# Kernel tuning notes

Hardware: AMD Instinct MI355X
Metric: run time of the kernel (lower is better)

Reference implementation:

```python
import jax, jax.numpy as jnp
import numpy as np

B, S, D = 128, 256, 768          # batch, seq (pre-sentinel), encoder dim
ARC, TAG = 500, 100              # arc / tag representation dims
LAYERS, TOPK = 2, 8              # config['gnn_layers'], config['top_k']
SP = S + 1                       # seq_len after head sentinel


def setup_inputs() -> dict:
    key = jax.random.key(0)
    ks = jax.random.split(key, 32)
    sc = 0.02
    inp = {
        'inputs': jax.random.normal(ks[0], (B, S, D), jnp.float32),
        'tag_embeddings': jax.random.randint(ks[1], (B, S), 0, 50),
        'mask': jnp.ones((B, S), jnp.int32),
        'head_indices': jax.random.randint(ks[2], (B, S), 0, S),
        'head_tags': jax.random.randint(ks[3], (B, S), 0, 50),
        # parameters
        'head_sentinel': jax.random.normal(ks[4], (D,), jnp.float32),
        'W_ha': jax.random.normal(ks[5], (D, ARC)) * sc, 'b_ha': jnp.zeros((ARC,)),
        'W_da': jax.random.normal(ks[6], (D, ARC)) * sc, 'b_da': jnp.zeros((ARC,)),
        'W_ht': jax.random.normal(ks[7], (D, TAG)) * sc, 'b_ht': jnp.zeros((TAG,)),
        'W_dt': jax.random.normal(ks[8], (D, TAG)) * sc, 'b_dt': jnp.zeros((TAG,)),
        # bilinear attention: use_input_biases=True -> (ARC+1, ARC+1), plus scalar bias
        'bil_W': jax.random.normal(ks[9], (LAYERS + 1, ARC + 1, ARC + 1)) * sc,
        'bil_b': jnp.zeros((LAYERS + 1,)),
        # GCNConv params (PyG: x @ W, symmetric-normalized aggregate, + bias)
        'c1a_W': jax.random.normal(ks[10], (ARC, ARC)) * sc, 'c1a_b': jnp.zeros((ARC,)),
        'c2a_W': jax.random.normal(ks[11], (ARC, ARC)) * sc, 'c2a_b': jnp.zeros((ARC,)),
        'c1r_W': jax.random.normal(ks[12], (TAG, TAG)) * sc, 'c1r_b': jnp.zeros((TAG,)),
        'c2r_W': jax.random.normal(ks[13], (TAG, TAG)) * sc, 'c2r_b': jnp.zeros((TAG,)),
    }
    return inp


def bilinear_attn(m1, m2, W, b):
    # AllenNLP BilinearMatrixAttention with use_input_biases=True
    ones1 = jnp.ones(m1.shape[:-1] + (1,), m1.dtype)
    m1b = jnp.concatenate([m1, ones1], -1)
    m2b = jnp.concatenate([m2, ones1], -1)
    return jnp.einsum('bie,ef,bjf->bij', m1b, W, m2b) + b


def batch_top_k(probs, k):
    # probs: [B, SP, SP] row-softmaxed; edge j(head)->i(dep) for each row's top-k cols,
    # with global (batched) node indexing.
    vals, idx = jax.lax.top_k(probs, k)                      # [B, SP, k]
    offs = (jnp.arange(B) * SP)[:, None, None]
    src = (idx + offs).reshape(-1)
    dst = (jnp.broadcast_to(jnp.arange(SP)[None, :, None], idx.shape) + offs).reshape(-1)
    return src, dst, vals.reshape(-1)


def gcn_conv(x, src, dst, ew, W, b):
    # PyG GCNConv: x@W, add self-loops (weight 1), sym norm, scatter-add at dst, + bias
    N = x.shape[0]
    x = x @ W
    loop = jnp.arange(N)
    row = jnp.concatenate([src, loop])
    col = jnp.concatenate([dst, loop])
    w = jnp.concatenate([ew, jnp.ones((N,), x.dtype)])
    deg = jax.ops.segment_sum(w, col, num_segments=N)
    dinv = jnp.where(deg > 0, jax.lax.rsqrt(deg), 0.0)
    norm = dinv[row] * w * dinv[col]
    out = jax.ops.segment_sum(x[row] * norm[:, None], col, num_segments=N)
    return out + b


def reference(inputs, tag_embeddings, mask, head_indices, head_tags,
              head_sentinel, W_ha, b_ha, W_da, b_da, W_ht, b_ht, W_dt, b_dt,
              bil_W, bil_b, c1a_W, c1a_b, c2a_W, c2a_b, c1r_W, c1r_b, c2r_W, c2r_b):
    elu = jax.nn.elu
    x = jnp.concatenate([jnp.broadcast_to(head_sentinel, (B, 1, D)), inputs], axis=1)  # [B,SP,D]
    head_arc = elu(x @ W_ha + b_ha)
    dept_arc = elu(x @ W_da + b_da)
    head_tag = elu(x @ W_ht + b_ht)
    dep_tag = elu(x @ W_dt + b_dt)

    def two_conv(feat, W1, b1, W2, b2, src, dst, ew):
        h = gcn_conv(feat.reshape(B * SP, -1), src, dst, ew, W1, b1)
        h = gcn_conv(elu(h), src, dst, ew, W2, b2)
        return h.reshape(B, SP, -1)

    for k in range(LAYERS):
        arc_logits = bilinear_attn(head_arc, dept_arc, bil_W[k], bil_b[k])
        arc_probs = jax.nn.softmax(arc_logits, axis=-1)
        src, dst, ew = batch_top_k(arc_probs, TOPK)
        head_arc = two_conv(head_arc, c1a_W, c1a_b, c2a_W, c2a_b, src, dst, ew)
        dept_arc = two_conv(dept_arc, c1a_W, c1a_b, c2a_W, c2a_b, src, dst, ew)
        head_tag = two_conv(head_tag, c1r_W, c1r_b, c2r_W, c2r_b, src, dst, ew)
        dep_tag = two_conv(dep_tag, c1r_W, c1r_b, c2r_W, c2r_b, src, dst, ew)

    arc_logits = bilinear_attn(head_arc, dept_arc, bil_W[-1], bil_b[-1])
    return arc_logits, head_tag, dep_tag
```

## Files before the change

### kernel.cpp

```cpp
#include <hip/hip_runtime.h>
#include <hip/hip_bf16.h>
#include <math.h>
#include <cstddef>

namespace {

constexpr int kB   = 128;
constexpr int kS   = 256;
constexpr int kD   = 768;
constexpr int kSP  = 257;
constexpr int kN   = kB * kSP;
constexpr int kARC = 500;
constexpr int kTAG = 100;
constexpr int KA   = 512;
constexpr int KT   = 128;
constexpr int NPA  = 1024;
constexpr int NPT  = 256;

typedef __attribute__((ext_vector_type(8))) short short8;
typedef __attribute__((ext_vector_type(4))) float floatx4;
typedef __attribute__((ext_vector_type(2))) float floatx2;
typedef __attribute__((ext_vector_type(4))) unsigned short ushort4v;
typedef __attribute__((ext_vector_type(2))) unsigned short ushort2v;
typedef __hip_bfloat16 bf;

__device__ __forceinline__ float bfval(bf h) { return __bfloat162float(h); }
__device__ __forceinline__ unsigned short bfbits(bf h) {
  unsigned short u; __builtin_memcpy(&u, &h, 2); return u;
}
__device__ __forceinline__ void splitf(float x, bf* h, bf* l) {
  bf hh = __float2bfloat16(x);
  *h = hh;
  *l = __float2bfloat16(x - __bfloat162float(hh));
}

__device__ __forceinline__ int swz8(int lid, int total) {
  int q = total >> 3, r = total & 7;
  int c = lid & 7, p = lid >> 3;
  return (c < r ? c * (q + 1) : r * (q + 1) + (c - r) * q) + p;
}

__device__ __forceinline__ void gload16(const bf* g, bf* l) {
  __builtin_amdgcn_global_load_lds(
      (const __attribute__((address_space(1))) void*)g,
      (__attribute__((address_space(3))) void*)l, 16, 0, 0);
}

__global__ void zerofill(unsigned* __restrict__ p, long n4) {
  long i = (long)blockIdx.x * 256 + threadIdx.x;
  if (i < n4) p[i] = 0u;
}

__global__ void detect_dtype_n(const unsigned* __restrict__ raw, int* __restrict__ flag,
                               int nwords) {
  int lane = threadIdx.x;
  int ok = 0, nz = 0;
  if (lane < nwords) {
    unsigned w = raw[lane];
    if (w != 0u) {
      nz = 1;
      int e = (w >> 7) & 0xFF;
      ok = (e >= 90 && e <= 140);
    }
  }
  unsigned long long ball_ok = __ballot(ok);
  unsigned long long ball_nz = __ballot(nz);
  if (lane == 0) {
    int cok = __popcll(ball_ok), cnz = __popcll(ball_nz);
    flag[0] = (cok * 4 >= cnz * 3) ? 1 : 0;
  }
}

__device__ __forceinline__ float rawload(const void* p, size_t i, int bfm) {
  return bfm ? __bfloat162float(((const bf*)p)[i]) : ((const float*)p)[i];
}

__global__ void conv_off(const void* __restrict__ src, float* __restrict__ dst,
                         int n, long off, const int* __restrict__ flag) {
  int i = blockIdx.x * 256 + threadIdx.x;
  if (i >= n) return;
  dst[i] = rawload(src, (size_t)off + i, *flag);
}

__global__ void wsplit_t(const void* __restrict__ src, const int* __restrict__ flag,
                         long srcOff, int ldsrc, int K, int N, int Kpad,
                         bf* __restrict__ Wh, bf* __restrict__ Wl) {
  long idx = (long)blockIdx.x * 256 + threadIdx.x;
  if (idx >= (long)N * Kpad) return;
  int n = (int)(idx / Kpad), k = (int)(idx % Kpad);
  float v = (k < K) ? rawload(src, (size_t)srcOff + (size_t)k * ldsrc + n, *flag) : 0.f;
  bf h, l;
  splitf(v, &h, &l);
  Wh[idx] = h; Wl[idx] = l;
}

__global__ void xsplit(const void* __restrict__ inp, const void* __restrict__ sent,
                       const int* __restrict__ fi, const int* __restrict__ fs,
                       bf* __restrict__ xh, bf* __restrict__ xl, int g0, int NG) {
  long idx = (long)blockIdx.x * 256 + threadIdx.x;
  long tot = (long)NG * (kD / 4);
  if (idx >= tot) return;
  int n = (int)(idx / (kD / 4));
  int k = (int)(idx % (kD / 4)) * 4;
  int b = n / kSP, r = n - b * kSP;
  const void* src;
  size_t base;
  int bfm;
  if (r == 0) { src = sent; base = (size_t)k; bfm = *fs; }
  else {
    src = inp;
    base = ((size_t)((g0 + b) * kS + (r - 1))) * kD + k;
    bfm = *fi;
  }
  float v[4];
  if (bfm) {
    ushort4v s = *(const ushort4v*)((const unsigned short*)src + base);
#pragma unroll
    for (int j = 0; j < 4; ++j) {
      bf h; unsigned short u = s[j];
      __builtin_memcpy(&h, &u, 2);
      v[j] = __bfloat162float(h);
    }
  } else {
    floatx4 f4 = *(const floatx4*)((const float*)src + base);
#pragma unroll
    for (int j = 0; j < 4; ++j) v[j] = f4[j];
  }
  ushort4v h4, l4;
#pragma unroll
  for (int j = 0; j < 4; ++j) {
    bf h, l;
    splitf(v[j], &h, &l);
    h4[j] = bfbits(h); l4[j] = bfbits(l);
  }
  size_t o = (size_t)n * kD + k;
  *(ushort4v*)((unsigned short*)xh + o) = h4;
  *(ushort4v*)((unsigned short*)xl + o) = l4;
}

constexpr int BM = 128, BN = 128, BK = 32;

template <int EPI, int OUTF32>
__global__ __launch_bounds__(256) void gemm_sp(
    const bf* __restrict__ Ah, const bf* __restrict__ Al, int lda,
    const bf* __restrict__ Bh, const bf* __restrict__ Bl, int ldb,
    bf* __restrict__ Ch, bf* __restrict__ Cl, float* __restrict__ Cf, int ldc,
    int M, int N, int K, const float* __restrict__ bias) {
  __shared__ bf sAh[2][BM][BK];
  __shared__ bf sAl[2][BM][BK];
  __shared__ bf sBh[2][BN][BK];
  __shared__ bf sBl[2][BN][BK];
  const int tid = threadIdx.x;
  const int lane = tid & 63, wave = tid >> 6;
  const int quad = lane >> 4, l15 = lane & 15;
  const int wm = (wave >> 1) * 64, wn = (wave & 1) * 64;
  const int gy = gridDim.y;
  const int sw = swz8(blockIdx.x + blockIdx.y * gridDim.x, gridDim.x * gy);
  const int m0 = (sw / gy) * BM, n0 = (sw % gy) * BN;
  const int lrow = lane >> 2, lkof = (lane & 3) * 8;

  const bf *pAh[2], *pAl[2], *pBh[2], *pBl[2];
  int rb[2];
#pragma unroll
  for (int jj = 0; jj < 2; ++jj) {
    rb[jj] = wave * 32 + jj * 16;
    int gm = m0 + rb[jj] + lrow; if (gm > M - 1) gm = M - 1;
    int gn = n0 + rb[jj] + lrow; if (gn > N - 1) gn = N - 1;
    pAh[jj] = Ah + (size_t)gm * lda + lkof;
    pAl[jj] = Al + (size_t)gm * lda + lkof;
    pBh[jj] = Bh + (size_t)gn * ldb + lkof;
    pBl[jj] = Bl + (size_t)gn * ldb + lkof;
  }

  auto stage = [&](int bi, int k0) {
#pragma unroll
    for (int jj = 0; jj < 2; ++jj) {
      gload16(pAh[jj] + k0, &sAh[bi][rb[jj]][0]);
      gload16(pAl[jj] + k0, &sAl[bi][rb[jj]][0]);
      gload16(pBh[jj] + k0, &sBh[bi][rb[jj]][0]);
      gload16(pBl[jj] + k0, &sBl[bi][rb[jj]][0]);
    }
  };

  floatx4 acc[4][4] = {};
  stage(0, 0);
  int cur = 0;
  for (int k0 = 0; k0 < K; k0 += BK) {
    __syncthreads();
    if (k0 + BK < K) stage(cur ^ 1, k0 + BK);
    short8 a_h[4], a_l[4], b_h[4], b_l[4];
#pragma unroll
    for (int t = 0; t < 4; ++t) {
      a_h[t] = *(const short8*)&sAh[cur][wm + t * 16 + l15][quad * 8];
      a_l[t] = *(const short8*)&sAl[cur][wm + t * 16 + l15][quad * 8];
      b_h[t] = *(const short8*)&sBh[cur][wn + t * 16 + l15][quad * 8];
      b_l[t] = *(const short8*)&sBl[cur][wn + t * 16 + l15][quad * 8];
    }
#pragma unroll
    for (int mt = 0; mt < 4; ++mt)
#pragma unroll
      for (int nt = 0; nt < 4; ++nt) {
        acc[mt][nt] = __builtin_amdgcn_mfma_f32_16x16x32_bf16(a_h[mt], b_h[nt], acc[mt][nt], 0, 0, 0);
        acc[mt][nt] = __builtin_amdgcn_mfma_f32_16x16x32_bf16(a_h[mt], b_l[nt], acc[mt][nt], 0, 0, 0);
        acc[mt][nt] = __builtin_amdgcn_mfma_f32_16x16x32_bf16(a_l[mt], b_h[nt], acc[mt][nt], 0, 0, 0);
      }
    cur ^= 1;
  }
#pragma unroll
  for (int mt = 0; mt < 4; ++mt)
#pragma unroll
    for (int reg = 0; reg < 4; ++reg) {
      int m = m0 + wm + mt * 16 + quad * 4 + reg;
      if (m >= M) continue;
#pragma unroll
      for (int nt = 0; nt < 4; ++nt) {
        int n = n0 + wn + nt * 16 + l15;
        if (OUTF32) {
          if (n < N) {
            float v = acc[mt][nt][reg];
            if (EPI >= 1) v += bias[n];
            if (EPI == 1) v = v > 0.f ? v : expm1f(v);
            Cf[(size_t)m * ldc + n] = v;
          }
        } else {
          size_t o = (size_t)m * ldc + n;
          if (n < N) {
            float v = acc[mt][nt][reg];
            if (EPI >= 1) v += bias[n];
            if (EPI == 1) v = v > 0.f ? v : expm1f(v);
            bf h, l;
            splitf(v, &h, &l);
            Ch[o] = h; Cl[o] = l;
          } else if (n < ldc) {
            Ch[o] = __float2bfloat16(0.f);
            Cl[o] = __float2bfloat16(0.f);
          }
        }
      }
    }
}

__global__ __launch_bounds__(256) void bilnt_sp(
    const bf* __restrict__ Th, const bf* __restrict__ Tl,
    const bf* __restrict__ Fh, const bf* __restrict__ Fl, int ldf,
    float* __restrict__ out, const float* __restrict__ bilb, int bidx,
    int g0, int globOut) {
  __shared__ bf sAh[2][BM][BK];
  __shared__ bf sAl[2][BM][BK];
  __shared__ bf sBh[2][BN][BK];
  __shared__ bf sBl[2][BN][BK];
  const int tid = threadIdx.x;
  const int lane = tid & 63, wave = tid >> 6;
  const int quad = lane >> 4, l15 = lane & 15;
  const int wm = (wave >> 1) * 64, wn = (wave & 1) * 64;
  const int gx = gridDim.x, gxy = gridDim.x * gridDim.y;
  const int sw = swz8(blockIdx.x + gx * blockIdx.y + gxy * blockIdx.z, gxy * gridDim.z);
  const int z = sw / gxy;
  const int rem = sw % gxy;
  const int m0 = (rem % gx) * BM, n0 = (rem / gx) * BN;
  const int lrow = lane >> 2, lkof = (lane & 3) * 8;
  const bf* Ah = Th + (size_t)z * kSP * KA;
  const bf* Al = Tl + (size_t)z * kSP * KA;
  const bf* Bh = Fh + (size_t)z * kSP * ldf;
  const bf* Bl = Fl + (size_t)z * kSP * ldf;

  const bf *pAh[2], *pAl[2], *pBh[2], *pBl[2];
  int rb[2];
#pragma unroll
  for (int jj = 0; jj < 2; ++jj) {
    rb[jj] = wave * 32 + jj * 16;
    int gm = m0 + rb[jj] + lrow; if (gm > kSP - 1) gm = kSP - 1;
    int gn = n0 + rb[jj] + lrow; if (gn > kSP - 1) gn = kSP - 1;
    pAh[jj] = Ah + (size_t)gm * KA + lkof;
    pAl[jj] = Al + (size_t)gm * KA + lkof;
    pBh[jj] = Bh + (size_t)gn * ldf + lkof;
    pBl[jj] = Bl + (size_t)gn * ldf + lkof;
  }

  auto stage = [&](int bi, int k0) {
#pragma unroll
    for (int jj = 0; jj < 2; ++jj) {
      gload16(pAh[jj] + k0, &sAh[bi][rb[jj]][0]);
      gload16(pAl[jj] + k0, &sAl[bi][rb[jj]][0]);
      gload16(pBh[jj] + k0, &sBh[bi][rb[jj]][0]);
      gload16(pBl[jj] + k0, &sBl[bi][rb[jj]][0]);
    }
  };

  floatx4 acc[4][4] = {};
  stage(0, 0);
  int cur = 0;
  for (int k0 = 0; k0 < KA; k0 += BK) {
    __syncthreads();
    if (k0 + BK < KA) stage(cur ^ 1, k0 + BK);
    short8 a_h[4], a_l[4], b_h[4], b_l[4];
#pragma unroll
    for (int t = 0; t < 4; ++t) {
      a_h[t] = *(const short8*)&sAh[cur][wm + t * 16 + l15][quad * 8];
      a_l[t] = *(const short8*)&sAl[cur][wm + t * 16 + l15][quad * 8];
      b_h[t] = *(const short8*)&sBh[cur][wn + t * 16 + l15][quad * 8];
      b_l[t] = *(const short8*)&sBl[cur][wn + t * 16 + l15][quad * 8];
    }
#pragma unroll
    for (int mt = 0; mt < 4; ++mt)
#pragma unroll
      for (int nt = 0; nt < 4; ++nt) {
        acc[mt][nt] = __builtin_amdgcn_mfma_f32_16x16x32_bf16(a_h[mt], b_h[nt], acc[mt][nt], 0, 0, 0);
        acc[mt][nt] = __builtin_amdgcn_mfma_f32_16x16x32_bf16(a_h[mt], b_l[nt], acc[mt][nt], 0, 0, 0);
        acc[mt][nt] = __builtin_amdgcn_mfma_f32_16x16x32_bf16(a_l[mt], b_h[nt], acc[mt][nt], 0, 0, 0);
      }
    cur ^= 1;
  }
  const float sb = bilb[bidx];
  const int bb = globOut ? (g0 + z) : z;
#pragma unroll
  for (int mt = 0; mt < 4; ++mt)
#pragma unroll
    for (int reg = 0; reg < 4; ++reg) {
      int i = m0 + wm + mt * 16 + quad * 4 + reg;
      if (i >= kSP) continue;
      float rowterm = bfval(Ah[(size_t)i * KA + 500]) + bfval(Al[(size_t)i * KA + 500]) + sb;
#pragma unroll
      for (int nt = 0; nt < 4; ++nt) {
        int j = n0 + wn + nt * 16 + l15;
        if (j >= kSP) continue;
        out[((size_t)bb * kSP + i) * kSP + j] = acc[mt][nt][reg] + rowterm;
      }
    }
}

__global__ void softmax_topk(const float* __restrict__ logits,
                             unsigned short* __restrict__ idx8,
                             float* __restrict__ val8,
                             float* __restrict__ dinv) {
  const int row = blockIdx.x;
  const int lane = threadIdx.x;
  const float* L = logits + (size_t)row * kSP;
  float v[5];
  int c[5];
#pragma unroll
  for (int q = 0; q < 5; ++q) {
    int j = lane + q * 64;
    c[q] = j;
    v[q] = (j < kSP) ? L[j] : -INFINITY;
  }
  float m = v[0];
#pragma unroll
  for (int q = 1; q < 5; ++q) m = fmaxf(m, v[q]);
  for (int off = 32; off > 0; off >>= 1) m = fmaxf(m, __shfl_xor(m, off));
  float s = 0.f;
#pragma unroll
  for (int q = 0; q < 5; ++q) s += expf(v[q] - m);
  for (int off = 32; off > 0; off >>= 1) s += __shfl_xor(s, off);
  const float invs = 1.f / s;
  float degsum = 0.f;
  for (int t = 0; t < 8; ++t) {
    float bvv = -INFINITY;
    int bii = 0;
#pragma unroll
    for (int q = 0; q < 5; ++q)
      if (v[q] > bvv) { bvv = v[q]; bii = c[q]; }
    for (int off = 32; off > 0; off >>= 1) {
      float ov = __shfl_xor(bvv, off);
      int oi = __shfl_xor(bii, off);
      if (ov > bvv || (ov == bvv && oi < bii)) { bvv = ov; bii = oi; }
    }
    float p = expf(bvv - m) * invs;
    degsum += p;
    if (lane == 0) { idx8[row * 8 + t] = (unsigned short)bii; val8[row * 8 + t] = p; }
#pragma unroll
    for (int q = 0; q < 5; ++q)
      if (c[q] == bii) v[q] = -INFINITY;
  }
  if (lane == 0) dinv[row] = 1.f / sqrtf(1.f + degsum);
}

template <int ELU, int OUTF32>
__global__ void gcn_agg(const float* __restrict__ Y, int ldy, int F,
                        const unsigned short* __restrict__ idx8,
                        const float* __restrict__ val8,
                        const float* __restrict__ dinv, const float* __restrict__ bias,
                        bf* __restrict__ Zh, bf* __restrict__ Zl,
                        float* __restrict__ Zf, int ldzf, long halfStr) {
  const int r = swz8(blockIdx.x, gridDim.x);
  const int m = r >> 1, p = r & 1;
  __shared__ float w[9];
  __shared__ int srcs[8];
  const int t = threadIdx.x;
  if (t < 8) {
    int b0 = m - (m % kSP);
    int s = b0 + (int)idx8[m * 8 + t];
    srcs[t] = 2 * s + p;
    w[t] = dinv[m] * val8[m * 8 + t] * dinv[s];
  } else if (t == 8) {
    float di = dinv[m];
    w[8] = di * di;
  }
  __syncthreads();
  const int lim = OUTF32 ? F : ldy;
  for (int f = t * 2; f < lim; f += (int)blockDim.x * 2) {
    size_t on = (size_t)r * ldy + f;
    if (!OUTF32 && f >= F) {
      ushort2v zz = {0, 0};
      *(ushort2v*)((unsigned short*)Zh + on) = zz;
      *(ushort2v*)((unsigned short*)Zl + on) = zz;
      continue;
    }
    floatx2 y0 = *(const floatx2*)(Y + on);
    float a0 = w[8] * y0[0], a1 = w[8] * y0[1];
#pragma unroll
    for (int e = 0; e < 8; ++e) {
      floatx2 ys = *(const floatx2*)(Y + (size_t)srcs[e] * ldy + f);
      a0 += w[e] * ys[0];
      a1 += w[e] * ys[1];
    }
    a0 += bias[f];
    a1 += bias[f + 1];
    if (ELU) {
      a0 = a0 > 0.f ? a0 : expm1f(a0);
      a1 = a1 > 0.f ? a1 : expm1f(a1);
    }
    if (OUTF32) {
      float* zp = Zf + (size_t)p * halfStr + (size_t)m * ldzf + f;
      floatx2 o = {a0, a1};
      *(floatx2*)zp = o;
    } else {
      bf h0, l0, h1, l1;
      splitf(a0, &h0, &l0);
      splitf(a1, &h1, &l1);
      ushort2v hv = {bfbits(h0), bfbits(h1)};
      ushort2v lv = {bfbits(l0), bfbits(l1)};
      *(ushort2v*)((unsigned short*)Zh + on) = hv;
      *(ushort2v*)((unsigned short*)Zl + on) = lv;
    }
  }
}

}

extern "C" void kernel_launch(void* const* d_in, const int* in_sizes, int n_in,
                              void* d_out, int out_size, void* d_ws, size_t ws_size,
                              hipStream_t stream) {
  (void)out_size;

  const int roleSize[20] = {kB * kS * kD, kD,
                            kD * kARC, kARC, kD * kARC, kARC,
                            kD * kTAG, kTAG, kD * kTAG, kTAG,
                            3 * 501 * 501, 3,
                            kARC * kARC, kARC, kARC * kARC, kARC,
                            kTAG * kTAG, kTAG, kTAG * kTAG, kTAG};
  const int roleOcc[20]  = {0, 0, 0, 0, 1, 1, 0, 0, 1, 1, 0, 0,
                            0, 2, 1, 3, 0, 2, 1, 3};
  int roleIdx[20] = {0, 5, 6, 7, 8, 9, 10, 11, 12, 13, 14, 15,
                     16, 17, 18, 19, 20, 21, 22, 23};
  for (int r = 0; r < 20; ++r) {
    int occ = 0, found = -1;
    for (int i = 0; i < n_in; ++i) {
      if (in_sizes[i] == roleSize[r]) {
        if (occ == roleOcc[r]) { found = i; break; }
        ++occ;
      }
    }
    if (found >= 0) roleIdx[r] = found;
    else if (roleIdx[r] >= n_in) roleIdx[r] = 0;
  }
  const void* src_of[20];
  for (int r = 0; r < 20; ++r) src_of[r] = d_in[roleIdx[r]];

  auto r1_bytes = [](size_t NG) -> size_t {
    size_t a = (size_t)2 * NG * KA * 4;
    size_t b = NG * kD * 2 * 2;
    size_t c = NG * KA * 2 * 2 + NG * kSP * 4;
    size_t m = a; if (b > m) m = b; if (c > m) m = c;
    return m;
  };
  auto need_bytes = [&](int GB) -> size_t {
    size_t NG = (size_t)GB * kSP, s = 0;
    auto al = [&](size_t b) { s += (b + 255) & ~(size_t)255; };
    al(256);
    al((size_t)NPA * kD * 2); al((size_t)NPA * kD * 2);
    al((size_t)NPT * kD * 2); al((size_t)NPT * kD * 2);
    al(NPA * 4); al(NPT * 4);
    for (int i = 0; i < 6; ++i) al((size_t)501 * KA * 2);
    al(3 * 501 * 4); al(256);
    for (int i = 0; i < 4; ++i) al((size_t)kARC * KA * 2);
    for (int i = 0; i < 4; ++i) al((size_t)kTAG * KT * 2);
    al(kARC * 4); al(kARC * 4); al(kTAG * 4); al(kTAG * 4);
    al(NG * NPA * 2); al(NG * NPA * 2);
    al(NG * NPT * 2); al(NG * NPT * 2);
    al(r1_bytes(NG));
    al((size_t)2 * NG * KA * 2 * 2);
    al(NG * 8 * 2); al(NG * 8 * 4); al(NG * 4);
    return s;
  };
  int GB = 1;
  for (int cand : {128, 64, 32, 16, 8, 4, 2, 1})
    if (need_bytes(cand) <= ws_size) { GB = cand; break; }
  const int G = kB / GB;
  const int NG = GB * kSP;
  const int mb  = (NG + BM - 1) / BM;
  const int mb2 = (2 * NG + BM - 1) / BM;

  char* ws = (char*)d_ws;
  size_t off = 0;
  auto alloc = [&](size_t bytes) -> void* {
    void* p = ws + off;
    off += (bytes + 255) & ~(size_t)255;
    return p;
  };
  int* flags = (int*)alloc(256);
  bf *WtABh = (bf*)alloc((size_t)NPA * kD * 2), *WtABl = (bf*)alloc((size_t)NPA * kD * 2);
  bf *WtTBh = (bf*)alloc((size_t)NPT * kD * 2), *WtTBl = (bf*)alloc((size_t)NPT * kD * 2);
  float* bpa = (float*)alloc(NPA * 4);
  float* bpt = (float*)alloc(NPT * 4);
  bf* bilWh[3]; bf* bilWl[3];
  for (int k = 0; k < 3; ++k) {
    bilWh[k] = (bf*)alloc((size_t)501 * KA * 2);
    bilWl[k] = (bf*)alloc((size_t)501 * KA * 2);
  }
  float* brow = (float*)alloc(3 * 501 * 4);
  float* bilbf = (float*)alloc(256);
  bf *c1ah = (bf*)alloc((size_t)kARC * KA * 2), *c1al = (bf*)alloc((size_t)kARC * KA * 2);
  bf *c2ah = (bf*)alloc((size_t)kARC * KA * 2), *c2al = (bf*)alloc((size_t)kARC * KA * 2);
  bf *c1rh = (bf*)alloc((size_t)kTAG * KT * 2), *c1rl = (bf*)alloc((size_t)kTAG * KT * 2);
  bf *c2rh = (bf*)alloc((size_t)kTAG * KT * 2), *c2rl = (bf*)alloc((size_t)kTAG * KT * 2);
  float* c1ab = (float*)alloc(kARC * 4);
  float* c2ab = (float*)alloc(kARC * 4);
  float* c1rb = (float*)alloc(kTAG * 4);
  float* c2rb = (float*)alloc(kTAG * 4);
  bf *FAh = (bf*)alloc((size_t)NG * NPA * 2), *FAl = (bf*)alloc((size_t)NG * NPA * 2);
  bf *FTh = (bf*)alloc((size_t)NG * NPT * 2), *FTl = (bf*)alloc((size_t)NG * NPT * 2);
  char* R1 = (char*)alloc(r1_bytes((size_t)NG));
  bf* xh = (bf*)R1;
  bf* xl = xh + (size_t)NG * kD;
  bf* Th = (bf*)R1;
  bf* Tl = Th + (size_t)NG * KA;
  float* logits = (float*)(R1 + (size_t)NG * KA * 2 * 2);
  float* Yf = (float*)R1;
  bf* Z2h = (bf*)alloc((size_t)2 * NG * KA * 2 * 2);
  bf* Z2l = Z2h + (size_t)2 * NG * KA;
  unsigned short* idx8 = (unsigned short*)alloc((size_t)NG * 8 * 2);
  float* val8 = (float*)alloc((size_t)NG * 8 * 4);
  float* dinv = (float*)alloc((size_t)NG * 4);

  for (int r = 0; r < 20; ++r) {
    int n = roleSize[r];
    int nwords = n / 4; if (nwords < 1) nwords = 1; if (nwords > 64) nwords = 64;
    detect_dtype_n<<<1, 64, 0, stream>>>((const unsigned*)src_of[r], flags + r, nwords);
  }
  auto cvt = [&](int role, float* dst, int n, long o) {
    conv_off<<<(n + 255) / 256, 256, 0, stream>>>(src_of[role], dst, n, o, flags + role);
  };
  auto wsp = [&](int role, long o, int ldsrc, int K, int N, int Kpad, bf* Wh, bf* Wl) {
    long tot = (long)N * Kpad;
    wsplit_t<<<(int)((tot + 255) / 256), 256, 0, stream>>>(src_of[role], flags + role, o,
                                                           ldsrc, K, N, Kpad, Wh, Wl);
  };
  auto zf = [&](void* p, size_t bytes) {
    long n4 = (long)(bytes / 4);
    zerofill<<<(int)((n4 + 255) / 256), 256, 0, stream>>>((unsigned*)p, n4);
  };

  zf(WtABh, (size_t)NPA * kD * 2); zf(WtABl, (size_t)NPA * kD * 2);
  zf(WtTBh, (size_t)NPT * kD * 2); zf(WtTBl, (size_t)NPT * kD * 2);
  zf(bpa, NPA * 4); zf(bpt, NPT * 4);
  wsp(2, 0, kARC, kD, kARC, kD, WtABh, WtABl);
  wsp(4, 0, kARC, kD, kARC, kD, WtABh + (size_t)KA * kD, WtABl + (size_t)KA * kD);
  wsp(6, 0, kTAG, kD, kTAG, kD, WtTBh, WtTBl);
  wsp(8, 0, kTAG, kD, kTAG, kD, WtTBh + (size_t)KT * kD, WtTBl + (size_t)KT * kD);
  cvt(3, bpa, kARC, 0); cvt(5, bpa + KA, kARC, 0);
  cvt(7, bpt, kTAG, 0); cvt(9, bpt + KT, kTAG, 0);
  cvt(11, bilbf, 3, 0);
  cvt(13, c1ab, kARC, 0); cvt(15, c2ab, kARC, 0); cvt(17, c1rb, kTAG, 0); cvt(19, c2rb, kTAG, 0);
  for (int k = 0; k < 3; ++k) {
    wsp(10, (long)k * 501 * 501, 501, 500, 501, KA, bilWh[k], bilWl[k]);
    cvt(10, brow + k * 501, 501, (long)k * 501 * 501 + 500 * 501);
  }
  wsp(12, 0, kARC, kARC, kARC, KA, c1ah, c1al);
  wsp(14, 0, kARC, kARC, kARC, KA, c2ah, c2al);
  wsp(16, 0, kTAG, kTAG, kTAG, KT, c1rh, c1rl);
  wsp(18, 0, kTAG, kTAG, kTAG, KT, c2rh, c2rl);

  float* outp = (float*)d_out;
  const size_t arc_elems = (size_t)kB * kSP * kSP;

  for (int g = 0; g < G; ++g) {
    const int g0 = g * GB;

    {
      long tot = (long)NG * (kD / 4);
      xsplit<<<(int)((tot + 255) / 256), 256, 0, stream>>>(
          src_of[0], src_of[1], flags + 0, flags + 1, xh, xl, g0, NG);
    }
    gemm_sp<1, 0><<<dim3(mb, NPA / BN), 256, 0, stream>>>(
        xh, xl, kD, WtABh, WtABl, kD, FAh, FAl, nullptr, NPA, NG, NPA, kD, bpa);
    gemm_sp<1, 0><<<dim3(mb, NPT / BN), 256, 0, stream>>>(
        xh, xl, kD, WtTBh, WtTBl, kD, FTh, FTl, nullptr, NPT, NG, NPT, kD, bpt);

    for (int k = 0; k < 2; ++k) {
      gemm_sp<2, 0><<<dim3(mb, 4), 256, 0, stream>>>(
          FAh, FAl, NPA, bilWh[k], bilWl[k], KA, Th, Tl, nullptr, KA, NG, 501, KA,
          brow + k * 501);
      bilnt_sp<<<dim3(3, 3, GB), 256, 0, stream>>>(
          Th, Tl, FAh + KA, FAl + KA, NPA, logits, bilbf, k, g0, 0);
      softmax_topk<<<NG, 64, 0, stream>>>(logits, idx8, val8, dinv);

      gemm_sp<0, 1><<<dim3(mb2, 4), 256, 0, stream>>>(
          FAh, FAl, KA, c1ah, c1al, KA, nullptr, nullptr, Yf, KA, 2 * NG, kARC, KA, nullptr);
      gcn_agg<1, 0><<<2 * NG, 256, 0, stream>>>(Yf, KA, kARC, idx8, val8, dinv, c1ab,
                                                Z2h, Z2l, nullptr, 0, 0);
      gemm_sp<0, 1><<<dim3(mb2, 4), 256, 0, stream>>>(
          Z2h, Z2l, KA, c2ah, c2al, KA, nullptr, nullptr, Yf, KA, 2 * NG, kARC, KA, nullptr);
      gcn_agg<0, 0><<<2 * NG, 256, 0, stream>>>(Yf, KA, kARC, idx8, val8, dinv, c2ab,
                                                FAh, FAl, nullptr, 0, 0);

      gemm_sp<0, 1><<<dim3(mb2, 1), 256, 0, stream>>>(
          FTh, FTl, KT, c1rh, c1rl, KT, nullptr, nullptr, Yf, KT, 2 * NG, kTAG, KT, nullptr);
      gcn_agg<1, 0><<<2 * NG, 64, 0, stream>>>(Yf, KT, kTAG, idx8, val8, dinv, c1rb,
                                               Z2h, Z2l, nullptr, 0, 0);
      gemm_sp<0, 1><<<dim3(mb2, 1), 256, 0, stream>>>(
          Z2h, Z2l, KT, c2rh, c2rl, KT, nullptr, nullptr, Yf, KT, 2 * NG, kTAG, KT, nullptr);
      if (k == 1) {
        float* dst = outp + arc_elems + (size_t)g0 * kSP * kTAG;
        gcn_agg<0, 1><<<2 * NG, 64, 0, stream>>>(Yf, KT, kTAG, idx8, val8, dinv, c2rb,
                                                 nullptr, nullptr, dst, kTAG,
                                                 (long)kN * kTAG);
      } else {
        gcn_agg<0, 0><<<2 * NG, 64, 0, stream>>>(Yf, KT, kTAG, idx8, val8, dinv, c2rb,
                                                 FTh, FTl, nullptr, 0, 0);
      }
    }

    gemm_sp<2, 0><<<dim3(mb, 4), 256, 0, stream>>>(
        FAh, FAl, NPA, bilWh[2], bilWl[2], KA, Th, Tl, nullptr, KA, NG, 501, KA,
        brow + 2 * 501);
    bilnt_sp<<<dim3(3, 3, GB), 256, 0, stream>>>(
        Th, Tl, FAh + KA, FAl + KA, NPA, outp, bilbf, 2, g0, 1);
  }
}
```

Measured before the change: 2.741 ms.

## Add triple-buffered 256x128 GEMM kernel with 8 waves for projection and GCN GEMMs

Introduces gemm_pipe, a 512-thread GEMM with a 256x128 output tile and a three-stage shared-memory ring. It issues loads two K-steps ahead and waits on partial vmcnt, so global loads overlap the MFMA work of the split-bf16 three-product accumulation. The encoder projections and all four GCN weight GEMMs now use it. The larger tile roughly triples LDS use and raises register pressure, which can lower occupancy. The 128-wide tag GEMMs also waste more rows at the M edge.

```diff
diff --git a/kernel.cpp b/kernel.cpp
--- a/kernel.cpp
+++ b/kernel.cpp
@@ -240,6 +240,119 @@
     }
 }
 
+template <int EPI, int OUTF32>
+__global__ __launch_bounds__(512) void gemm_pipe(
+    const bf* __restrict__ Ah, const bf* __restrict__ Al, int lda,
+    const bf* __restrict__ Bh, const bf* __restrict__ Bl, int ldb,
+    bf* __restrict__ Ch, bf* __restrict__ Cl, float* __restrict__ Cf, int ldc,
+    int M, int N, int K, const float* __restrict__ bias) {
+  __shared__ bf sAh[3][256][BK];
+  __shared__ bf sAl[3][256][BK];
+  __shared__ bf sBh[3][128][BK];
+  __shared__ bf sBl[3][128][BK];
+  const int tid = threadIdx.x;
+  const int lane = tid & 63, wave = tid >> 6;
+  const int quad = lane >> 4, l15 = lane & 15;
+  const int wm = (wave >> 1) * 64, wn = (wave & 1) * 64;
+  const int gy = gridDim.y;
+  const int sw = swz8(blockIdx.x + blockIdx.y * gridDim.x, gridDim.x * gy);
+  const int m0 = (sw / gy) * 256, n0 = (sw % gy) * 128;
+  const int lrow = lane >> 2, lkof = (lane & 3) * 8;
+
+  const bf *pA0[2], *pA1[2], *pB0, *pB1;
+  int ra[2];
+#pragma unroll
+  for (int j = 0; j < 2; ++j) {
+    ra[j] = wave * 32 + j * 16;
+    int gm = m0 + ra[j] + lrow; if (gm > M - 1) gm = M - 1;
+    pA0[j] = Ah + (size_t)gm * lda + lkof;
+    pA1[j] = Al + (size_t)gm * lda + lkof;
+  }
+  const int rbw = wave * 16;
+  {
+    int gn = n0 + rbw + lrow; if (gn > N - 1) gn = N - 1;
+    pB0 = Bh + (size_t)gn * ldb + lkof;
+    pB1 = Bl + (size_t)gn * ldb + lkof;
+  }
+
+  auto stage = [&](int bi, int k0) {
+#pragma unroll
+    for (int j = 0; j < 2; ++j) {
+      gload16(pA0[j] + k0, &sAh[bi][ra[j]][0]);
+      gload16(pA1[j] + k0, &sAl[bi][ra[j]][0]);
+    }
+    gload16(pB0 + k0, &sBh[bi][rbw][0]);
+    gload16(pB1 + k0, &sBl[bi][rbw][0]);
+  };
+
+  floatx4 acc[4][4] = {};
+  stage(0, 0);
+  if (BK < K) stage(1, BK);
+  int cur = 0;
+  for (int k0 = 0; k0 < K; k0 += BK) {
+    if (k0 + BK < K) {
+      asm volatile("s_waitcnt vmcnt(6)" ::: "memory");
+    } else {
+      asm volatile("s_waitcnt vmcnt(0)" ::: "memory");
+    }
+    __builtin_amdgcn_s_barrier();
+    __builtin_amdgcn_sched_barrier(0);
+    if (k0 + 2 * BK < K) {
+      int nb = cur + 2; if (nb >= 3) nb -= 3;
+      stage(nb, k0 + 2 * BK);
+    }
+    short8 a_h[4], a_l[4], b_h[4], b_l[4];
+#pragma unroll
+    for (int t = 0; t < 4; ++t) {
+      a_h[t] = *(const short8*)&sAh[cur][wm + t * 16 + l15][quad * 8];
+      a_l[t] = *(const short8*)&sAl[cur][wm + t * 16 + l15][quad * 8];
+      b_h[t] = *(const short8*)&sBh[cur][wn + t * 16 + l15][quad * 8];
+      b_l[t] = *(const short8*)&sBl[cur][wn + t * 16 + l15][quad * 8];
+    }
+#pragma unroll
+    for (int mt = 0; mt < 4; ++mt)
+#pragma unroll
+      for (int nt = 0; nt < 4; ++nt) {
+        acc[mt][nt] = __builtin_amdgcn_mfma_f32_16x16x32_bf16(a_h[mt], b_h[nt], acc[mt][nt], 0, 0, 0);
+        acc[mt][nt] = __builtin_amdgcn_mfma_f32_16x16x32_bf16(a_h[mt], b_l[nt], acc[mt][nt], 0, 0, 0);
+        acc[mt][nt] = __builtin_amdgcn_mfma_f32_16x16x32_bf16(a_l[mt], b_h[nt], acc[mt][nt], 0, 0, 0);
+      }
+    ++cur; if (cur == 3) cur = 0;
+  }
+#pragma unroll
+  for (int mt = 0; mt < 4; ++mt)
+#pragma unroll
+    for (int reg = 0; reg < 4; ++reg) {
+      int m = m0 + wm + mt * 16 + quad * 4 + reg;
+      if (m >= M) continue;
+#pragma unroll
+      for (int nt = 0; nt < 4; ++nt) {
+        int n = n0 + wn + nt * 16 + l15;
+        if (OUTF32) {
+          if (n < N) {
+            float v = acc[mt][nt][reg];
+            if (EPI >= 1) v += bias[n];
+            if (EPI == 1) v = v > 0.f ? v : expm1f(v);
+            Cf[(size_t)m * ldc + n] = v;
+          }
+        } else {
+          size_t o = (size_t)m * ldc + n;
+          if (n < N) {
+            float v = acc[mt][nt][reg];
+            if (EPI >= 1) v += bias[n];
+            if (EPI == 1) v = v > 0.f ? v : expm1f(v);
+            bf h, l;
+            splitf(v, &h, &l);
+            Ch[o] = h; Cl[o] = l;
+          } else if (n < ldc) {
+            Ch[o] = __float2bfloat16(0.f);
+            Cl[o] = __float2bfloat16(0.f);
+          }
+        }
+      }
+    }
+}
+
 __global__ __launch_bounds__(256) void bilnt_sp(
     const bf* __restrict__ Th, const bf* __restrict__ Tl,
     const bf* __restrict__ Fh, const bf* __restrict__ Fl, int ldf,
@@ -498,8 +611,9 @@
     if (need_bytes(cand) <= ws_size) { GB = cand; break; }
   const int G = kB / GB;
   const int NG = GB * kSP;
-  const int mb  = (NG + BM - 1) / BM;
-  const int mb2 = (2 * NG + BM - 1) / BM;
+  const int mb   = (NG + BM - 1) / BM;
+  const int mbp  = (NG + 255) / 256;
+  const int mbp2 = (2 * NG + 255) / 256;
 
   char* ws = (char*)d_ws;
   size_t off = 0;
@@ -592,9 +706,9 @@
       xsplit<<<(int)((tot + 255) / 256), 256, 0, stream>>>(
           src_of[0], src_of[1], flags + 0, flags + 1, xh, xl, g0, NG);
     }
-    gemm_sp<1, 0><<<dim3(mb, NPA / BN), 256, 0, stream>>>(
+    gemm_pipe<1, 0><<<dim3(mbp, NPA / 128), 512, 0, stream>>>(
         xh, xl, kD, WtABh, WtABl, kD, FAh, FAl, nullptr, NPA, NG, NPA, kD, bpa);
-    gemm_sp<1, 0><<<dim3(mb, NPT / BN), 256, 0, stream>>>(
+    gemm_pipe<1, 0><<<dim3(mbp, NPT / 128), 512, 0, stream>>>(
         xh, xl, kD, WtTBh, WtTBl, kD, FTh, FTl, nullptr, NPT, NG, NPT, kD, bpt);
 
     for (int k = 0; k < 2; ++k) {
@@ -605,20 +719,20 @@
           Th, Tl, FAh + KA, FAl + KA, NPA, logits, bilbf, k, g0, 0);
       softmax_topk<<<NG, 64, 0, stream>>>(logits, idx8, val8, dinv);
 
-      gemm_sp<0, 1><<<dim3(mb2, 4), 256, 0, stream>>>(
+      gemm_pipe<0, 1><<<dim3(mbp2, (kARC + 127) / 128), 512, 0, stream>>>(
           FAh, FAl, KA, c1ah, c1al, KA, nullptr, nullptr, Yf, KA, 2 * NG, kARC, KA, nullptr);
       gcn_agg<1, 0><<<2 * NG, 256, 0, stream>>>(Yf, KA, kARC, idx8, val8, dinv, c1ab,
                                                 Z2h, Z2l, nullptr, 0, 0);
-      gemm_sp<0, 1><<<dim3(mb2, 4), 256, 0, stream>>>(
+      gemm_pipe<0, 1><<<dim3(mbp2, (kARC + 127) / 128), 512, 0, stream>>>(
           Z2h, Z2l, KA, c2ah, c2al, KA, nullptr, nullptr, Yf, KA, 2 * NG, kARC, KA, nullptr);
       gcn_agg<0, 0><<<2 * NG, 256, 0, stream>>>(Yf, KA, kARC, idx8, val8, dinv, c2ab,
                                                 FAh, FAl, nullptr, 0, 0);
 
-      gemm_sp<0, 1><<<dim3(mb2, 1), 256, 0, stream>>>(
+      gemm_pipe<0, 1><<<dim3(mbp2, 1), 512, 0, stream>>>(
           FTh, FTl, KT, c1rh, c1rl, KT, nullptr, nullptr, Yf, KT, 2 * NG, kTAG, KT, nullptr);
       gcn_agg<1, 0><<<2 * NG, 64, 0, stream>>>(Yf, KT, kTAG, idx8, val8, dinv, c1rb,
                                                Z2h, Z2l, nullptr, 0, 0);
-      gemm_sp<0, 1><<<dim3(mb2, 1), 256, 0, stream>>>(
+      gemm_pipe<0, 1><<<dim3(mbp2, 1), 512, 0, stream>>>(
           Z2h, Z2l, KT, c2rh, c2rl, KT, nullptr, nullptr, Yf, KT, 2 * NG, kTAG, KT, nullptr);
       if (k == 1) {
         float* dst = outp + arc_elems + (size_t)g0 * kSP * kTAG;
```

Result: slower. 2.978 ms (+8.7%).
